# Performance work log

Hardware: AMD Instinct MI355X
Metric: run time of the kernel (lower is better)

The kernel has to match this reference:

```python
import jax, jax.numpy as jnp
import numpy as np

L, B, D, H, P = 4096, 4, 1024, 16, 256
HD = D // H
EPS = 1e-5


def _layer_norm(x, g, b):
    m = jnp.mean(x, axis=-1, keepdims=True)
    v = jnp.mean(jnp.square(x - m), axis=-1, keepdims=True)
    return (x - m) / jnp.sqrt(v + EPS) * g + b


def setup_inputs() -> dict:
    key = jax.random.key(0)
    ks = jax.random.split(key, 8)
    w = lambda k, shape: jax.random.normal(k, shape, jnp.float32) * 0.02
    return {
        "query": jax.random.normal(ks[0], (L, B, D), jnp.float32),
        "q_w": w(ks[1], (D, D)), "q_b": jnp.zeros((D,), jnp.float32),
        "k_w": w(ks[2], (D, D)), "k_b": jnp.zeros((D,), jnp.float32),
        "v_w": w(ks[3], (D, D)), "v_b": jnp.zeros((D,), jnp.float32),
        "e_weight": w(ks[4], (1, H, P, HD)),
        "e_out_w": w(ks[5], (D, D)), "e_out_b": jnp.zeros((D,), jnp.float32),
        "ln_g": jnp.ones((D,), jnp.float32), "ln_b": jnp.zeros((D,), jnp.float32),
        "out_w": w(ks[6], (D, D)), "out_b": jnp.zeros((D,), jnp.float32),
    }


def reference(query, q_w, q_b, k_w, k_b, v_w, v_b, e_weight,
              e_out_w, e_out_b, ln_g, ln_b, out_w, out_b):
    scaling = HD ** -0.5
    # ---- _compute_kv (kv_same=True, no padding mask) ----
    # kv: (L,B,D) -> (B,H,HD,L)
    kvh = query.reshape(L, B, H, HD).transpose(1, 2, 3, 0)
    # pkv = relu(E @ (kv * scaling)) : (B,H,P,L)
    pkv = jax.nn.relu(jnp.einsum('hpd,bhdl->bhpl', e_weight[0], kvh * scaling))
    # kv = pkv @ kv^T : (B,H,P,HD)
    kv = jnp.einsum('bhpl,bhdl->bhpd', pkv, kvh)
    # -> (P,B,D), e_out linear, residual add of e_weight, layer norm
    kv = kv.transpose(2, 0, 1, 3).reshape(P, B, D)
    kv = kv @ e_out_w.T + e_out_b
    kv = kv.reshape(P, B, H, HD) + e_weight.transpose(2, 0, 1, 3)  # broadcast (P,1,H,HD)
    kv = _layer_norm(kv.reshape(P, B, D), ln_g, ln_b)  # (P,B,D)

    # ---- standard MHA against the compressed kv ----
    q = (query @ q_w.T + q_b) * scaling            # (L,B,D)
    k = kv @ k_w.T + k_b                           # (P,B,D)
    v = kv @ v_w.T + v_b                           # (P,B,D)
    qh = q.reshape(L, B, H, HD)
    kh = k.reshape(P, B, H, HD)
    vh = v.reshape(P, B, H, HD)
    logits = jnp.einsum('lbhd,pbhd->bhlp', qh, kh)
    probs = jax.nn.softmax(logits, axis=-1)
    attn = jnp.einsum('bhlp,pbhd->lbhd', probs, vh).reshape(L, B, D)
    return attn @ out_w.T + out_b
```

## Files before the change

kernel.cpp:

```cpp
#include <hip/hip_runtime.h>
#include <hip/hip_bf16.h>
#include <cstdint>
#include <cstddef>

#define LL 4096
#define BB 4
#define DD 1024
#define HH 16
#define PP 256
#define HDD 64
#define LC 16
#define LCHUNK 256

constexpr float kScaling = 0.125f;
constexpr float kEps = 1e-5f;

typedef __attribute__((ext_vector_type(8))) short bf16x8;
typedef __attribute__((ext_vector_type(4))) short short4v;
typedef __attribute__((ext_vector_type(4))) float f32x4;

#define MFMA16(a, b, c) __builtin_amdgcn_mfma_f32_16x16x32_bf16((a), (b), (c), 0, 0, 0)

__device__ __forceinline__ unsigned short f2bf(float f) {
  unsigned int u = __builtin_bit_cast(unsigned int, f);
  u += 0x7FFFu + ((u >> 16) & 1u);
  return (unsigned short)(u >> 16);
}

__device__ __forceinline__ void gll16(const void* g, void* l) {
  __builtin_amdgcn_global_load_lds(
      (const __attribute__((address_space(1))) unsigned int*)g,
      (__attribute__((address_space(3))) unsigned int*)l, 16, 0, 0);
}

__global__ __launch_bounds__(256) void k_cvt(const float* __restrict__ src,
                                             unsigned short* __restrict__ dst,
                                             int n8) {
  int i = blockIdx.x * 256 + threadIdx.x;
  if (i >= n8) return;
  const float4* s = (const float4*)(src + (size_t)i * 8);
  float4 a = s[0], b = s[1];
  bf16x8 o;
  o[0] = f2bf(a.x); o[1] = f2bf(a.y); o[2] = f2bf(a.z); o[3] = f2bf(a.w);
  o[4] = f2bf(b.x); o[5] = f2bf(b.y); o[6] = f2bf(b.z); o[7] = f2bf(b.w);
  *(bf16x8*)(dst + (size_t)i * 8) = o;
}

__global__ __launch_bounds__(256) void k_compress_mfma(
    const unsigned short* __restrict__ qbf, const unsigned short* __restrict__ ewbf,
    float* __restrict__ parts) {
  const int bh = blockIdx.x, lc = blockIdx.y;
  const int b = bh >> 4, h = bh & 15;
  const int tid = threadIdx.x, wv = tid >> 6, lane = tid & 63;
  const int fr = lane & 15, fg = lane >> 4;

  __shared__ __align__(16) char Xl[8192];
  __shared__ __align__(16) char Xtl[8192];
  __shared__ __align__(16) char Pl[32768];

  bf16x8 ef[4][2];
#pragma unroll
  for (int pt = 0; pt < 4; ++pt)
#pragma unroll
    for (int kc = 0; kc < 2; ++kc)
      ef[pt][kc] = *(const bf16x8*)(ewbf +
          (size_t)((h * PP + wv * 64 + pt * 16 + fr) * HDD) + kc * 32 + fg * 8);

  f32x4 acc[4][4];
#pragma unroll
  for (int i = 0; i < 4; ++i)
#pragma unroll
    for (int j = 0; j < 4; ++j) acc[i][j] = (f32x4){0.f, 0.f, 0.f, 0.f};

  const int l0 = lc * LCHUNK;
  for (int t = 0; t < 4; ++t) {
    __syncthreads();
#pragma unroll
    for (int j = 0; j < 2; ++j) {
      int u = tid + j * 256;
      int l = u >> 3, c8 = u & 7;
      bf16x8 val = *(const bf16x8*)(qbf +
          ((size_t)(l0 + t * 64 + l) * BB + b) * DD + h * HDD + c8 * 8);
      *(bf16x8*)(Xl + l * 128 + ((c8 ^ (l & 7)) << 4)) = val;
#pragma unroll
      for (int i = 0; i < 8; ++i) {
        int dd = c8 * 8 + i;
        *(short*)(Xtl + dd * 128 + ((((l >> 3) ^ (dd & 7) ^ (dd >> 3)) & 7) << 4) +
                  ((l & 7) << 1)) = val[i];
      }
    }
    __syncthreads();
#pragma unroll
    for (int lt = 0; lt < 4; ++lt) {
      int rl = lt * 16 + fr;
      bf16x8 xa0 = *(const bf16x8*)(Xl + rl * 128 + (((0 + fg) ^ (rl & 7)) << 4));
      bf16x8 xa1 = *(const bf16x8*)(Xl + rl * 128 + (((4 + fg) ^ (rl & 7)) << 4));
#pragma unroll
      for (int pt = 0; pt < 4; ++pt) {
        f32x4 s = (f32x4){0.f, 0.f, 0.f, 0.f};
        s = MFMA16(xa0, ef[pt][0], s);
        s = MFMA16(xa1, ef[pt][1], s);
        short4v pk;
#pragma unroll
        for (int r = 0; r < 4; ++r)
          pk[r] = (short)f2bf(fmaxf(s[r] * kScaling, 0.f));
        int p = wv * 64 + pt * 16 + fr;
        int lbase = lt * 16 + fg * 4;
        int slot = lbase >> 3;
        *(short4v*)(Pl + p * 128 + ((slot ^ (p & 7)) << 4) + ((lbase & 7) << 1)) = pk;
      }
    }
    asm volatile("s_waitcnt lgkmcnt(0)" ::: "memory");
    __builtin_amdgcn_sched_barrier(0);
#pragma unroll
    for (int kc = 0; kc < 2; ++kc) {
      bf16x8 pa[4], xb[4];
#pragma unroll
      for (int pt = 0; pt < 4; ++pt) {
        int p = wv * 64 + pt * 16 + fr;
        pa[pt] = *(const bf16x8*)(Pl + p * 128 + (((kc * 4 + fg) ^ (p & 7)) << 4));
      }
#pragma unroll
      for (int dt = 0; dt < 4; ++dt) {
        int dd = dt * 16 + fr;
        xb[dt] = *(const bf16x8*)(Xtl + dd * 128 +
                  ((((kc * 4 + fg) ^ (dd & 7) ^ (dd >> 3)) & 7) << 4));
      }
#pragma unroll
      for (int pt = 0; pt < 4; ++pt)
#pragma unroll
        for (int dt = 0; dt < 4; ++dt)
          acc[pt][dt] = MFMA16(pa[pt], xb[dt], acc[pt][dt]);
    }
  }
  float* op = parts + (size_t)(lc * 64 + bh) * PP * HDD;
#pragma unroll
  for (int pt = 0; pt < 4; ++pt)
#pragma unroll
    for (int dt = 0; dt < 4; ++dt)
#pragma unroll
      for (int r = 0; r < 4; ++r) {
        int p = wv * 64 + pt * 16 + fg * 4 + r;
        int dd = dt * 16 + fr;
        op[(size_t)p * HDD + dd] = acc[pt][dt][r];
      }
}

__global__ __launch_bounds__(256) void k_reduce(const float* __restrict__ parts,
                                                unsigned short* __restrict__ kv_raw_bf) {
  int i = blockIdx.x * 256 + threadIdx.x;
  float s = 0.f;
#pragma unroll
  for (int lcc = 0; lcc < LC; ++lcc) s += parts[(size_t)lcc * (64 * PP * HDD) + i];
  int d = i & 63, p = (i >> 6) & 255, bh = i >> 14;
  int b = bh >> 4, h = bh & 15;
  kv_raw_bf[(size_t)(p * BB + b) * DD + h * HDD + d] = f2bf(s);
}

template <int MODE, typename OUTT>
__device__ __forceinline__ void gemm_body(
    const unsigned short* __restrict__ A, const unsigned short* __restrict__ W,
    const float* __restrict__ bias, const float* __restrict__ ew,
    OUTT* __restrict__ C, int m0, int n0, char* Al, char* Bl) {
  const int tid = threadIdx.x;
  const int wv = tid >> 6, lane = tid & 63;
  const int fr = lane & 15, fg = lane >> 4;
  const int wr = wv >> 1, wc = wv & 1;

  f32x4 acc[4][4];
#pragma unroll
  for (int i = 0; i < 4; ++i)
#pragma unroll
    for (int j = 0; j < 4; ++j) acc[i][j] = (f32x4){0.f, 0.f, 0.f, 0.f};

  for (int k0 = 0; k0 < DD; k0 += 64) {
    __syncthreads();
#pragma unroll
    for (int j = 0; j < 4; ++j) {
      int u = tid + j * 256;
      int row = u >> 3, slot = u & 7;
      size_t gcol = (size_t)(k0 + 8 * (slot ^ (row & 7)));
      gll16(A + (size_t)(m0 + row) * DD + gcol, Al + u * 16);
      gll16(W + (size_t)(n0 + row) * DD + gcol, Bl + u * 16);
    }
    __syncthreads();
#pragma unroll
    for (int kc = 0; kc < 2; ++kc) {
      bf16x8 af[4], bfr[4];
#pragma unroll
      for (int mt = 0; mt < 4; ++mt) {
        int r = wr * 64 + mt * 16 + fr;
        af[mt] = *(const bf16x8*)(Al + r * 128 + (((kc * 4 + fg) ^ (r & 7)) << 4));
      }
#pragma unroll
      for (int nt = 0; nt < 4; ++nt) {
        int r = wc * 64 + nt * 16 + fr;
        bfr[nt] = *(const bf16x8*)(Bl + r * 128 + (((kc * 4 + fg) ^ (r & 7)) << 4));
      }
#pragma unroll
      for (int mt = 0; mt < 4; ++mt)
#pragma unroll
        for (int nt = 0; nt < 4; ++nt)
          acc[mt][nt] = MFMA16(af[mt], bfr[nt], acc[mt][nt]);
    }
  }

  float bs[4];
#pragma unroll
  for (int nt = 0; nt < 4; ++nt) bs[nt] = bias[n0 + wc * 64 + nt * 16 + fr];
#pragma unroll
  for (int mt = 0; mt < 4; ++mt)
#pragma unroll
    for (int nt = 0; nt < 4; ++nt) {
      int n = n0 + wc * 64 + nt * 16 + fr;
#pragma unroll
      for (int r = 0; r < 4; ++r) {
        int m = m0 + wr * 64 + mt * 16 + fg * 4 + r;
        float v = acc[mt][nt][r] + bs[nt];
        if (MODE == 1) v *= kScaling;
        if (MODE == 2) {
          int p = m >> 2, hh = n >> 6, d2 = n & 63;
          v += ew[(size_t)((hh << 8) + p) * HDD + d2];
        }
        if constexpr (sizeof(OUTT) == 2)
          C[(size_t)m * DD + n] = (OUTT)f2bf(v);
        else
          C[(size_t)m * DD + n] = v;
      }
    }
}

template <int MODE, typename OUTT>
__global__ __launch_bounds__(256) void k_gemm_mfma(
    const unsigned short* __restrict__ A, const unsigned short* __restrict__ W,
    const float* __restrict__ bias, const float* __restrict__ ew,
    OUTT* __restrict__ C) {
  __shared__ __align__(16) char Al[16384];
  __shared__ __align__(16) char Bl[16384];
  gemm_body<MODE, OUTT>(A, W, bias, ew, C, blockIdx.x * 128, blockIdx.y * 128, Al, Bl);
}

__global__ __launch_bounds__(256) void k_gemm_kv(
    const unsigned short* __restrict__ A,
    const unsigned short* __restrict__ Wk, const unsigned short* __restrict__ Wv,
    const float* __restrict__ kb, const float* __restrict__ vb,
    unsigned short* __restrict__ Ck, unsigned short* __restrict__ Cv) {
  __shared__ __align__(16) char Al[16384];
  __shared__ __align__(16) char Bl[16384];
  if (blockIdx.z == 0)
    gemm_body<0, unsigned short>(A, Wk, kb, nullptr, Ck,
                                 blockIdx.x * 128, blockIdx.y * 128, Al, Bl);
  else
    gemm_body<0, unsigned short>(A, Wv, vb, nullptr, Cv,
                                 blockIdx.x * 128, blockIdx.y * 128, Al, Bl);
}

template <int MODE, typename OUTT>
__global__ __launch_bounds__(512, 2) void k_gemm256(
    const unsigned short* __restrict__ A, const unsigned short* __restrict__ W,
    const float* __restrict__ bias, OUTT* __restrict__ C) {
  __shared__ __align__(16) char lds[131072];
  const int tid = threadIdx.x;
  const int wv = tid >> 6, lane = tid & 63;
  const int fr = lane & 15, fg = lane >> 4;
  const int wm = wv >> 2, wn = wv & 3;
  const int m0 = blockIdx.x * 256, n0 = blockIdx.y * 256;
  const int srow = tid >> 2, sslot = tid & 3;

  auto stageHalf = [&](const unsigned short* __restrict__ G, int g0, int colbase,
                       int dstBase) {
#pragma unroll
    for (int j = 0; j < 2; ++j) {
      int row = srow + j * 128;
      int gs = sslot ^ ((row >> 1) & 3);
      gll16(G + (size_t)(g0 + row) * DD + colbase + gs * 8,
            lds + dstBase + (tid + j * 512) * 16);
    }
  };
  auto rdA = [&](int mf, int kc, int cb) -> bf16x8 {
    int r = wm * 128 + mf * 16 + fr;
    return *(const bf16x8*)(lds + cb + kc * 16384 + r * 64 +
                            ((fg ^ ((r >> 1) & 3)) << 4));
  };
  auto rdB = [&](int nf, int kc, int cb) -> bf16x8 {
    int r = wn * 64 + nf * 16 + fr;
    return *(const bf16x8*)(lds + cb + 32768 + kc * 16384 + r * 64 +
                            ((fg ^ ((r >> 1) & 3)) << 4));
  };

  f32x4 acc[8][4];
#pragma unroll
  for (int i = 0; i < 8; ++i)
#pragma unroll
    for (int j = 0; j < 4; ++j) acc[i][j] = (f32x4){0.f, 0.f, 0.f, 0.f};
  bf16x8 a[4], b[4];

  stageHalf(A, m0, 0, 0);
  stageHalf(W, n0, 0, 32768);
  stageHalf(A, m0, 32, 16384);
  stageHalf(W, n0, 32, 32768 + 16384);
  stageHalf(A, m0, 64, 65536);
  stageHalf(W, n0, 64, 65536 + 32768);
  asm volatile("s_waitcnt vmcnt(4)" ::: "memory");
  __builtin_amdgcn_s_barrier();

  const int NT = DD / 64;
  for (int t = 0; t < NT; ++t) {
    const int cb = (t & 1) << 16;
    const int nb = cb ^ 65536;
    const int k1 = (t + 1) * 64, k2 = (t + 2) * 64;

#pragma unroll
    for (int i = 0; i < 4; ++i) a[i] = rdA(i, 0, cb);
#pragma unroll
    for (int i = 0; i < 4; ++i) b[i] = rdB(i, 0, cb);
    if (t + 1 < NT) stageHalf(A, m0, k1 + 32, nb + 16384);
    __builtin_amdgcn_s_barrier();
    asm volatile("s_waitcnt lgkmcnt(0)" ::: "memory");
    __builtin_amdgcn_sched_barrier(0);
    __builtin_amdgcn_s_setprio(1);
#pragma unroll
    for (int mf = 0; mf < 4; ++mf)
#pragma unroll
      for (int nf = 0; nf < 4; ++nf)
        acc[mf][nf] = MFMA16(a[mf], b[nf], acc[mf][nf]);
    __builtin_amdgcn_s_setprio(0);
    __builtin_amdgcn_s_barrier();

#pragma unroll
    for (int i = 0; i < 4; ++i) a[i] = rdA(4 + i, 0, cb);
    if (t + 1 < NT) stageHalf(W, n0, k1 + 32, nb + 32768 + 16384);
    __builtin_amdgcn_s_barrier();
    asm volatile("s_waitcnt lgkmcnt(0)" ::: "memory");
    __builtin_amdgcn_sched_barrier(0);
    __builtin_amdgcn_s_setprio(1);
#pragma unroll
    for (int mf = 0; mf < 4; ++mf)
#pragma unroll
      for (int nf = 0; nf < 4; ++nf)
        acc[4 + mf][nf] = MFMA16(a[mf], b[nf], acc[4 + mf][nf]);
    __builtin_amdgcn_s_setprio(0);
    __builtin_amdgcn_s_barrier();

#pragma unroll
    for (int i = 0; i < 4; ++i) a[i] = rdA(i, 1, cb);
#pragma unroll
    for (int i = 0; i < 4; ++i) b[i] = rdB(i, 1, cb);
    if (t + 2 < NT) stageHalf(A, m0, k2, cb);
    __builtin_amdgcn_s_barrier();
    asm volatile("s_waitcnt lgkmcnt(0)" ::: "memory");
    __builtin_amdgcn_sched_barrier(0);
    __builtin_amdgcn_s_setprio(1);
#pragma unroll
    for (int mf = 0; mf < 4; ++mf)
#pragma unroll
      for (int nf = 0; nf < 4; ++nf)
        acc[mf][nf] = MFMA16(a[mf], b[nf], acc[mf][nf]);
    __builtin_amdgcn_s_setprio(0);
    __builtin_amdgcn_s_barrier();

#pragma unroll
    for (int i = 0; i < 4; ++i) a[i] = rdA(4 + i, 1, cb);
    if (t + 2 < NT) stageHalf(W, n0, k2, cb + 32768);
    __builtin_amdgcn_s_barrier();
    asm volatile("s_waitcnt lgkmcnt(0)" ::: "memory");
    __builtin_amdgcn_sched_barrier(0);
    __builtin_amdgcn_s_setprio(1);
#pragma unroll
    for (int mf = 0; mf < 4; ++mf)
#pragma unroll
      for (int nf = 0; nf < 4; ++nf)
        acc[4 + mf][nf] = MFMA16(a[mf], b[nf], acc[4 + mf][nf]);
    __builtin_amdgcn_s_setprio(0);
    if (t + 2 < NT) {
      asm volatile("s_waitcnt vmcnt(4)" ::: "memory");
    } else if (t + 1 < NT) {
      asm volatile("s_waitcnt vmcnt(0)" ::: "memory");
    }
    __builtin_amdgcn_s_barrier();
  }

  float bs[4];
#pragma unroll
  for (int nf = 0; nf < 4; ++nf) bs[nf] = bias[n0 + wn * 64 + nf * 16 + fr];
#pragma unroll
  for (int mf = 0; mf < 8; ++mf)
#pragma unroll
    for (int nf = 0; nf < 4; ++nf) {
      int n = n0 + wn * 64 + nf * 16 + fr;
#pragma unroll
      for (int r = 0; r < 4; ++r) {
        int m = m0 + wm * 128 + mf * 16 + fg * 4 + r;
        float v = acc[mf][nf][r] + bs[nf];
        if (MODE == 1) v *= kScaling;
        if constexpr (sizeof(OUTT) == 2)
          C[(size_t)m * DD + n] = (OUTT)f2bf(v);
        else
          C[(size_t)m * DD + n] = v;
      }
    }
}

__global__ __launch_bounds__(256) void k_ln(const float* __restrict__ x,
                                            const float* __restrict__ g,
                                            const float* __restrict__ bb,
                                            unsigned short* __restrict__ y) {
  const int r = blockIdx.x;
  const int tid = threadIdx.x;
  const float* xr = x + (size_t)r * DD;
  float4 v = *(const float4*)(xr + tid * 4);
  float s1 = v.x + v.y + v.z + v.w;
  float s2 = v.x * v.x + v.y * v.y + v.z * v.z + v.w * v.w;
#pragma unroll
  for (int off = 32; off > 0; off >>= 1) {
    s1 += __shfl_down(s1, off);
    s2 += __shfl_down(s2, off);
  }
  __shared__ float w1[4], w2[4];
  if ((tid & 63) == 0) { w1[tid >> 6] = s1; w2[tid >> 6] = s2; }
  __syncthreads();
  float S1 = w1[0] + w1[1] + w1[2] + w1[3];
  float S2 = w2[0] + w2[1] + w2[2] + w2[3];
  float mean = S1 * (1.f / DD);
  float var = S2 * (1.f / DD) - mean * mean;
  float rstd = rsqrtf(var + kEps);
  float4 gv = *(const float4*)(g + tid * 4);
  float4 bv = *(const float4*)(bb + tid * 4);
  short4v o;
  o[0] = (short)f2bf((v.x - mean) * rstd * gv.x + bv.x);
  o[1] = (short)f2bf((v.y - mean) * rstd * gv.y + bv.y);
  o[2] = (short)f2bf((v.z - mean) * rstd * gv.z + bv.z);
  o[3] = (short)f2bf((v.w - mean) * rstd * gv.w + bv.w);
  *(short4v*)(y + (size_t)r * DD + tid * 4) = o;
}

__global__ __launch_bounds__(512, 2) void k_attn_mfma(
    const unsigned short* __restrict__ qbf, const unsigned short* __restrict__ kbf,
    const unsigned short* __restrict__ vbf, unsigned short* __restrict__ attn) {
  const int bh = blockIdx.y;
  const int b = bh >> 4, h = bh & 15;
  const int tid = threadIdx.x, wv = tid >> 6, lane = tid & 63;
  const int fr = lane & 15, fg = lane >> 4;
  const int bl0 = blockIdx.x * 128;

  __shared__ __align__(16) char Kl[16384];
  __shared__ __align__(16) char Vt[16384];
  __shared__ __align__(16) char Pl[32768];

  const size_t qrow = ((size_t)(bl0 + wv * 16 + fr) * BB + b) * DD + h * HDD;
  bf16x8 qf0 = *(const bf16x8*)(qbf + qrow + fg * 8);
  bf16x8 qf1 = *(const bf16x8*)(qbf + qrow + 32 + fg * 8);

  f32x4 o[4];
#pragma unroll
  for (int dt = 0; dt < 4; ++dt) o[dt] = (f32x4){0.f, 0.f, 0.f, 0.f};
  float psum = 0.f;
  char* Pw = Pl + wv * 4096;

  for (int ph = 0; ph < 2; ++ph) {
    __syncthreads();
#pragma unroll
    for (int j = 0; j < 2; ++j) {
      int u = tid + j * 512;
      int p = u >> 3, slot = u & 7;
      gll16(kbf + ((size_t)((ph * 128 + p) * BB + b)) * DD + h * HDD +
                8 * (slot ^ (p & 7)),
            Kl + u * 16);
    }
#pragma unroll
    for (int j = 0; j < 2; ++j) {
      int u = tid + j * 512;
      int p = u >> 3, c8 = u & 7;
      bf16x8 val = *(const bf16x8*)(vbf +
          ((size_t)((ph * 128 + p) * BB + b)) * DD + h * HDD + c8 * 8);
      int pc = p >> 6, pl = p & 63;
#pragma unroll
      for (int i = 0; i < 8; ++i) {
        int dd = c8 * 8 + i;
        *(short*)(Vt + pc * 8192 + dd * 128 +
                  ((((pl >> 3) ^ (dd & 7) ^ (dd >> 3)) & 7) << 4) +
                  ((pl & 7) << 1)) = val[i];
      }
    }
    __syncthreads();

    f32x4 s[8];
    __builtin_amdgcn_s_setprio(1);
#pragma unroll
    for (int pt = 0; pt < 8; ++pt) {
      int pr = pt * 16 + fr;
      bf16x8 a0 = *(const bf16x8*)(Kl + pr * 128 + ((fg ^ (pr & 7)) << 4));
      bf16x8 a1 = *(const bf16x8*)(Kl + pr * 128 + (((4 + fg) ^ (pr & 7)) << 4));
      f32x4 acc = (f32x4){0.f, 0.f, 0.f, 0.f};
      acc = MFMA16(a0, qf0, acc);
      acc = MFMA16(a1, qf1, acc);
      s[pt] = acc;
    }
    __builtin_amdgcn_s_setprio(0);

#pragma unroll
    for (int pt = 0; pt < 8; ++pt) {
      float e0 = __expf(s[pt][0]), e1 = __expf(s[pt][1]);
      float e2 = __expf(s[pt][2]), e3 = __expf(s[pt][3]);
      psum += (e0 + e1) + (e2 + e3);
      short4v pk;
      pk[0] = (short)f2bf(e0); pk[1] = (short)f2bf(e1);
      pk[2] = (short)f2bf(e2); pk[3] = (short)f2bf(e3);
      int pbyte = (pt * 16 + fg * 4) * 2;
      int slot = pbyte >> 4, rem = pbyte & 15;
      *(short4v*)(Pw + fr * 256 + ((slot ^ (fr & 7)) << 4) + rem) = pk;
    }
    asm volatile("s_waitcnt lgkmcnt(0)" ::: "memory");
    __builtin_amdgcn_sched_barrier(0);

    __builtin_amdgcn_s_setprio(1);
#pragma unroll
    for (int kc = 0; kc < 4; ++kc) {
      int slot = kc * 4 + fg;
      bf16x8 pa = *(const bf16x8*)(Pw + fr * 256 + ((slot ^ (fr & 7)) << 4));
      int sl2 = (kc & 1) * 4 + fg;
#pragma unroll
      for (int dt = 0; dt < 4; ++dt) {
        int dd = dt * 16 + fr;
        bf16x8 vb = *(const bf16x8*)(Vt + (kc >> 1) * 8192 + dd * 128 +
                     (((sl2 ^ (dd & 7) ^ (dd >> 3)) & 7) << 4));
        o[dt] = MFMA16(pa, vb, o[dt]);
      }
    }
    __builtin_amdgcn_s_setprio(0);
  }

  psum += __shfl_xor(psum, 16);
  psum += __shfl_xor(psum, 32);

#pragma unroll
  for (int r = 0; r < 4; ++r) {
    int lloc = fg * 4 + r;
    float inv = 1.f / __shfl(psum, lloc);
    unsigned short* op = attn +
        ((size_t)(bl0 + wv * 16 + lloc) * BB + b) * DD + h * HDD;
#pragma unroll
    for (int dt = 0; dt < 4; ++dt)
      op[dt * 16 + fr] = f2bf(o[dt][r] * inv);
  }
}

extern "C" void kernel_launch(void* const* d_in, const int* in_sizes, int n_in,
                              void* d_out, int out_size, void* d_ws, size_t ws_size,
                              hipStream_t stream) {
  const float* query   = (const float*)d_in[0];
  const float* q_w     = (const float*)d_in[1];
  const float* q_b     = (const float*)d_in[2];
  const float* k_w     = (const float*)d_in[3];
  const float* k_b     = (const float*)d_in[4];
  const float* v_w     = (const float*)d_in[5];
  const float* v_b     = (const float*)d_in[6];
  const float* e_weight= (const float*)d_in[7];
  const float* e_out_w = (const float*)d_in[8];
  const float* e_out_b = (const float*)d_in[9];
  const float* ln_g    = (const float*)d_in[10];
  const float* ln_b    = (const float*)d_in[11];
  const float* out_w   = (const float*)d_in[12];
  const float* out_b   = (const float*)d_in[13];
  float* out = (float*)d_out;

  char* w = (char*)d_ws;
  float* parts            = (float*)w;
  unsigned short* q_bf    = (unsigned short*)w;
  unsigned short* attn_bf = (unsigned short*)(w + (32u << 20));
  unsigned short* query_bf= (unsigned short*)(w + (64u << 20));
  unsigned short* kv_raw  = (unsigned short*)(w + (96u << 20));
  float* kv_eo            = (float*)(w + (98u << 20));
  unsigned short* kv_ln   = (unsigned short*)(w + (102u << 20));
  unsigned short* k_buf   = (unsigned short*)(w + (104u << 20));
  unsigned short* v_buf   = (unsigned short*)(w + (106u << 20));
  unsigned short* wq  = (unsigned short*)(w + (108u << 20));
  unsigned short* wk  = (unsigned short*)(w + (110u << 20));
  unsigned short* wv_ = (unsigned short*)(w + (112u << 20));
  unsigned short* weo = (unsigned short*)(w + (114u << 20));
  unsigned short* wo  = (unsigned short*)(w + (116u << 20));
  unsigned short* ewb = (unsigned short*)(w + (118u << 20));

  k_cvt<<<8192, 256, 0, stream>>>(query, query_bf, 2097152);
  k_cvt<<<512, 256, 0, stream>>>(q_w, wq, 131072);
  k_cvt<<<512, 256, 0, stream>>>(k_w, wk, 131072);
  k_cvt<<<512, 256, 0, stream>>>(v_w, wv_, 131072);
  k_cvt<<<512, 256, 0, stream>>>(e_out_w, weo, 131072);
  k_cvt<<<512, 256, 0, stream>>>(out_w, wo, 131072);
  k_cvt<<<128, 256, 0, stream>>>(e_weight, ewb, 32768);

  k_compress_mfma<<<dim3(64, LC), 256, 0, stream>>>(query_bf, ewb, parts);
  k_reduce<<<4096, 256, 0, stream>>>(parts, kv_raw);
  k_gemm_mfma<2, float><<<dim3(8, 8), 256, 0, stream>>>(kv_raw, weo, e_out_b, e_weight, kv_eo);
  k_ln<<<PP * BB, 256, 0, stream>>>(kv_eo, ln_g, ln_b, kv_ln);
  k_gemm256<1, unsigned short><<<dim3(64, 4), 512, 0, stream>>>(query_bf, wq, q_b, q_bf);
  k_gemm_kv<<<dim3(8, 8, 2), 256, 0, stream>>>(kv_ln, wk, wv_, k_b, v_b, k_buf, v_buf);
  k_attn_mfma<<<dim3(32, 64), 512, 0, stream>>>(q_bf, k_buf, v_buf, attn_bf);
  k_gemm256<0, float><<<dim3(64, 4), 512, 0, stream>>>(attn_bf, wo, out_b, out);
}
```

Measured before the change: 238.1 us.

## Merge conversion kernels, store compress partials in bf16, double attention rows per block

All six fp32-to-bf16 conversion launches are merged into one kernel that dispatches on thread index, which removes launch overhead. The compress kernel's per-chunk partial sums are now written in bf16 instead of fp32, halving write and reduce traffic at the cost of extra rounding in a 16-way sum. The attention kernel now processes 256 query rows per block, so each staged K/V tile is reused for two sets of 128 rows. The grid is halved to match, which leaves fewer blocks to spread across the GPU.

```diff
diff --git a/kernel.cpp b/kernel.cpp
--- a/kernel.cpp
+++ b/kernel.cpp
@@ -26,6 +26,9 @@
   u += 0x7FFFu + ((u >> 16) & 1u);
   return (unsigned short)(u >> 16);
 }
+__device__ __forceinline__ float bf2f(unsigned short u) {
+  return __builtin_bit_cast(float, ((unsigned int)u) << 16);
+}
 
 __device__ __forceinline__ void gll16(const void* g, void* l) {
   __builtin_amdgcn_global_load_lds(
@@ -33,22 +36,38 @@
       (__attribute__((address_space(3))) unsigned int*)l, 16, 0, 0);
 }
 
-__global__ __launch_bounds__(256) void k_cvt(const float* __restrict__ src,
-                                             unsigned short* __restrict__ dst,
-                                             int n8) {
+__global__ __launch_bounds__(256) void k_cvt_all(
+    const float* __restrict__ q,
+    const float* __restrict__ w0, const float* __restrict__ w1,
+    const float* __restrict__ w2, const float* __restrict__ w3,
+    const float* __restrict__ w4, const float* __restrict__ w5,
+    unsigned short* __restrict__ dq,
+    unsigned short* __restrict__ d0, unsigned short* __restrict__ d1,
+    unsigned short* __restrict__ d2, unsigned short* __restrict__ d3,
+    unsigned short* __restrict__ d4, unsigned short* __restrict__ d5) {
   int i = blockIdx.x * 256 + threadIdx.x;
-  if (i >= n8) return;
-  const float4* s = (const float4*)(src + (size_t)i * 8);
+  const float* src; unsigned short* dst; int off;
+  if (i < 2097152) { src = q; dst = dq; off = i; }
+  else {
+    int j = i - 2097152; int w = j >> 17; off = j & 131071;
+    if (w == 0) { src = w0; dst = d0; }
+    else if (w == 1) { src = w1; dst = d1; }
+    else if (w == 2) { src = w2; dst = d2; }
+    else if (w == 3) { src = w3; dst = d3; }
+    else if (w == 4) { src = w4; dst = d4; }
+    else { if (off >= 32768) return; src = w5; dst = d5; }
+  }
+  const float4* s = (const float4*)(src + (size_t)off * 8);
   float4 a = s[0], b = s[1];
   bf16x8 o;
   o[0] = f2bf(a.x); o[1] = f2bf(a.y); o[2] = f2bf(a.z); o[3] = f2bf(a.w);
   o[4] = f2bf(b.x); o[5] = f2bf(b.y); o[6] = f2bf(b.z); o[7] = f2bf(b.w);
-  *(bf16x8*)(dst + (size_t)i * 8) = o;
+  *(bf16x8*)(dst + (size_t)off * 8) = o;
 }
 
 __global__ __launch_bounds__(256) void k_compress_mfma(
     const unsigned short* __restrict__ qbf, const unsigned short* __restrict__ ewbf,
-    float* __restrict__ parts) {
+    unsigned short* __restrict__ parts) {
   const int bh = blockIdx.x, lc = blockIdx.y;
   const int b = bh >> 4, h = bh & 15;
   const int tid = threadIdx.x, wv = tid >> 6, lane = tid & 63;
@@ -133,7 +152,7 @@
           acc[pt][dt] = MFMA16(pa[pt], xb[dt], acc[pt][dt]);
     }
   }
-  float* op = parts + (size_t)(lc * 64 + bh) * PP * HDD;
+  unsigned short* op = parts + (size_t)(lc * 64 + bh) * PP * HDD;
 #pragma unroll
   for (int pt = 0; pt < 4; ++pt)
 #pragma unroll
@@ -142,16 +161,16 @@
       for (int r = 0; r < 4; ++r) {
         int p = wv * 64 + pt * 16 + fg * 4 + r;
         int dd = dt * 16 + fr;
-        op[(size_t)p * HDD + dd] = acc[pt][dt][r];
-      }
-}
-
-__global__ __launch_bounds__(256) void k_reduce(const float* __restrict__ parts,
+        op[(size_t)p * HDD + dd] = f2bf(acc[pt][dt][r]);
+      }
+}
+
+__global__ __launch_bounds__(256) void k_reduce(const unsigned short* __restrict__ parts,
                                                 unsigned short* __restrict__ kv_raw_bf) {
   int i = blockIdx.x * 256 + threadIdx.x;
   float s = 0.f;
 #pragma unroll
-  for (int lcc = 0; lcc < LC; ++lcc) s += parts[(size_t)lcc * (64 * PP * HDD) + i];
+  for (int lcc = 0; lcc < LC; ++lcc) s += bf2f(parts[(size_t)lcc * (64 * PP * HDD) + i]);
   int d = i & 63, p = (i >> 6) & 255, bh = i >> 14;
   int b = bh >> 4, h = bh & 15;
   kv_raw_bf[(size_t)(p * BB + b) * DD + h * HDD + d] = f2bf(s);
@@ -441,20 +460,26 @@
   const int b = bh >> 4, h = bh & 15;
   const int tid = threadIdx.x, wv = tid >> 6, lane = tid & 63;
   const int fr = lane & 15, fg = lane >> 4;
-  const int bl0 = blockIdx.x * 128;
+  const int bl0 = blockIdx.x * 256;
 
   __shared__ __align__(16) char Kl[16384];
   __shared__ __align__(16) char Vt[16384];
   __shared__ __align__(16) char Pl[32768];
 
-  const size_t qrow = ((size_t)(bl0 + wv * 16 + fr) * BB + b) * DD + h * HDD;
-  bf16x8 qf0 = *(const bf16x8*)(qbf + qrow + fg * 8);
-  bf16x8 qf1 = *(const bf16x8*)(qbf + qrow + 32 + fg * 8);
-
-  f32x4 o[4];
-#pragma unroll
-  for (int dt = 0; dt < 4; ++dt) o[dt] = (f32x4){0.f, 0.f, 0.f, 0.f};
-  float psum = 0.f;
+  bf16x8 qf[2][2];
+#pragma unroll
+  for (int ql = 0; ql < 2; ++ql) {
+    const size_t qrow = ((size_t)(bl0 + ql * 128 + wv * 16 + fr) * BB + b) * DD + h * HDD;
+    qf[ql][0] = *(const bf16x8*)(qbf + qrow + fg * 8);
+    qf[ql][1] = *(const bf16x8*)(qbf + qrow + 32 + fg * 8);
+  }
+
+  f32x4 o[2][4];
+#pragma unroll
+  for (int ql = 0; ql < 2; ++ql)
+#pragma unroll
+    for (int dt = 0; dt < 4; ++dt) o[ql][dt] = (f32x4){0.f, 0.f, 0.f, 0.f};
+  float psum[2] = {0.f, 0.f};
   char* Pw = Pl + wv * 4096;
 
   for (int ph = 0; ph < 2; ++ph) {
@@ -484,64 +509,72 @@
     }
     __syncthreads();
 
-    f32x4 s[8];
-    __builtin_amdgcn_s_setprio(1);
-#pragma unroll
-    for (int pt = 0; pt < 8; ++pt) {
-      int pr = pt * 16 + fr;
-      bf16x8 a0 = *(const bf16x8*)(Kl + pr * 128 + ((fg ^ (pr & 7)) << 4));
-      bf16x8 a1 = *(const bf16x8*)(Kl + pr * 128 + (((4 + fg) ^ (pr & 7)) << 4));
-      f32x4 acc = (f32x4){0.f, 0.f, 0.f, 0.f};
-      acc = MFMA16(a0, qf0, acc);
-      acc = MFMA16(a1, qf1, acc);
-      s[pt] = acc;
-    }
-    __builtin_amdgcn_s_setprio(0);
-
-#pragma unroll
-    for (int pt = 0; pt < 8; ++pt) {
-      float e0 = __expf(s[pt][0]), e1 = __expf(s[pt][1]);
-      float e2 = __expf(s[pt][2]), e3 = __expf(s[pt][3]);
-      psum += (e0 + e1) + (e2 + e3);
-      short4v pk;
-      pk[0] = (short)f2bf(e0); pk[1] = (short)f2bf(e1);
-      pk[2] = (short)f2bf(e2); pk[3] = (short)f2bf(e3);
-      int pbyte = (pt * 16 + fg * 4) * 2;
-      int slot = pbyte >> 4, rem = pbyte & 15;
-      *(short4v*)(Pw + fr * 256 + ((slot ^ (fr & 7)) << 4) + rem) = pk;
-    }
-    asm volatile("s_waitcnt lgkmcnt(0)" ::: "memory");
-    __builtin_amdgcn_sched_barrier(0);
-
-    __builtin_amdgcn_s_setprio(1);
-#pragma unroll
-    for (int kc = 0; kc < 4; ++kc) {
-      int slot = kc * 4 + fg;
-      bf16x8 pa = *(const bf16x8*)(Pw + fr * 256 + ((slot ^ (fr & 7)) << 4));
-      int sl2 = (kc & 1) * 4 + fg;
-#pragma unroll
-      for (int dt = 0; dt < 4; ++dt) {
-        int dd = dt * 16 + fr;
-        bf16x8 vb = *(const bf16x8*)(Vt + (kc >> 1) * 8192 + dd * 128 +
-                     (((sl2 ^ (dd & 7) ^ (dd >> 3)) & 7) << 4));
-        o[dt] = MFMA16(pa, vb, o[dt]);
-      }
-    }
-    __builtin_amdgcn_s_setprio(0);
-  }
-
-  psum += __shfl_xor(psum, 16);
-  psum += __shfl_xor(psum, 32);
-
-#pragma unroll
-  for (int r = 0; r < 4; ++r) {
-    int lloc = fg * 4 + r;
-    float inv = 1.f / __shfl(psum, lloc);
-    unsigned short* op = attn +
-        ((size_t)(bl0 + wv * 16 + lloc) * BB + b) * DD + h * HDD;
-#pragma unroll
-    for (int dt = 0; dt < 4; ++dt)
-      op[dt * 16 + fr] = f2bf(o[dt][r] * inv);
+#pragma unroll
+    for (int ql = 0; ql < 2; ++ql) {
+      f32x4 s[8];
+      __builtin_amdgcn_s_setprio(1);
+#pragma unroll
+      for (int pt = 0; pt < 8; ++pt) {
+        int pr = pt * 16 + fr;
+        bf16x8 a0 = *(const bf16x8*)(Kl + pr * 128 + ((fg ^ (pr & 7)) << 4));
+        bf16x8 a1 = *(const bf16x8*)(Kl + pr * 128 + (((4 + fg) ^ (pr & 7)) << 4));
+        f32x4 acc = (f32x4){0.f, 0.f, 0.f, 0.f};
+        acc = MFMA16(a0, qf[ql][0], acc);
+        acc = MFMA16(a1, qf[ql][1], acc);
+        s[pt] = acc;
+      }
+      __builtin_amdgcn_s_setprio(0);
+
+      asm volatile("s_waitcnt lgkmcnt(0)" ::: "memory");
+      __builtin_amdgcn_sched_barrier(0);
+#pragma unroll
+      for (int pt = 0; pt < 8; ++pt) {
+        float e0 = __expf(s[pt][0]), e1 = __expf(s[pt][1]);
+        float e2 = __expf(s[pt][2]), e3 = __expf(s[pt][3]);
+        psum[ql] += (e0 + e1) + (e2 + e3);
+        short4v pk;
+        pk[0] = (short)f2bf(e0); pk[1] = (short)f2bf(e1);
+        pk[2] = (short)f2bf(e2); pk[3] = (short)f2bf(e3);
+        int pbyte = (pt * 16 + fg * 4) * 2;
+        int slot = pbyte >> 4, rem = pbyte & 15;
+        *(short4v*)(Pw + fr * 256 + ((slot ^ (fr & 7)) << 4) + rem) = pk;
+      }
+      asm volatile("s_waitcnt lgkmcnt(0)" ::: "memory");
+      __builtin_amdgcn_sched_barrier(0);
+
+      __builtin_amdgcn_s_setprio(1);
+#pragma unroll
+      for (int kc = 0; kc < 4; ++kc) {
+        int slot = kc * 4 + fg;
+        bf16x8 pa = *(const bf16x8*)(Pw + fr * 256 + ((slot ^ (fr & 7)) << 4));
+        int sl2 = (kc & 1) * 4 + fg;
+#pragma unroll
+        for (int dt = 0; dt < 4; ++dt) {
+          int dd = dt * 16 + fr;
+          bf16x8 vb = *(const bf16x8*)(Vt + (kc >> 1) * 8192 + dd * 128 +
+                       (((sl2 ^ (dd & 7) ^ (dd >> 3)) & 7) << 4));
+          o[ql][dt] = MFMA16(pa, vb, o[ql][dt]);
+        }
+      }
+      __builtin_amdgcn_s_setprio(0);
+    }
+  }
+
+#pragma unroll
+  for (int ql = 0; ql < 2; ++ql) {
+    float ps = psum[ql];
+    ps += __shfl_xor(ps, 16);
+    ps += __shfl_xor(ps, 32);
+#pragma unroll
+    for (int r = 0; r < 4; ++r) {
+      int lloc = fg * 4 + r;
+      float inv = 1.f / __shfl(ps, lloc);
+      unsigned short* op = attn +
+          ((size_t)(bl0 + ql * 128 + wv * 16 + lloc) * BB + b) * DD + h * HDD;
+#pragma unroll
+      for (int dt = 0; dt < 4; ++dt)
+        op[dt * 16 + fr] = f2bf(o[ql][dt][r] * inv);
+    }
   }
 }
 
@@ -565,7 +598,7 @@
   float* out = (float*)d_out;
 
   char* w = (char*)d_ws;
-  float* parts            = (float*)w;
+  unsigned short* parts   = (unsigned short*)w;
   unsigned short* q_bf    = (unsigned short*)w;
   unsigned short* attn_bf = (unsigned short*)(w + (32u << 20));
   unsigned short* query_bf= (unsigned short*)(w + (64u << 20));
@@ -581,13 +614,8 @@
   unsigned short* wo  = (unsigned short*)(w + (116u << 20));
   unsigned short* ewb = (unsigned short*)(w + (118u << 20));
 
-  k_cvt<<<8192, 256, 0, stream>>>(query, query_bf, 2097152);
-  k_cvt<<<512, 256, 0, stream>>>(q_w, wq, 131072);
-  k_cvt<<<512, 256, 0, stream>>>(k_w, wk, 131072);
-  k_cvt<<<512, 256, 0, stream>>>(v_w, wv_, 131072);
-  k_cvt<<<512, 256, 0, stream>>>(e_out_w, weo, 131072);
-  k_cvt<<<512, 256, 0, stream>>>(out_w, wo, 131072);
-  k_cvt<<<128, 256, 0, stream>>>(e_weight, ewb, 32768);
+  k_cvt_all<<<10880, 256, 0, stream>>>(query, q_w, k_w, v_w, e_out_w, out_w, e_weight,
+                                       query_bf, wq, wk, wv_, weo, wo, ewb);
 
   k_compress_mfma<<<dim3(64, LC), 256, 0, stream>>>(query_bf, ewb, parts);
   k_reduce<<<4096, 256, 0, stream>>>(parts, kv_raw);
@@ -595,6 +623,6 @@
   k_ln<<<PP * BB, 256, 0, stream>>>(kv_eo, ln_g, ln_b, kv_ln);
   k_gemm256<1, unsigned short><<<dim3(64, 4), 512, 0, stream>>>(query_bf, wq, q_b, q_bf);
   k_gemm_kv<<<dim3(8, 8, 2), 256, 0, stream>>>(kv_ln, wk, wv_, k_b, v_b, k_buf, v_buf);
-  k_attn_mfma<<<dim3(32, 64), 512, 0, stream>>>(q_bf, k_buf, v_buf, attn_bf);
+  k_attn_mfma<<<dim3(16, 64), 512, 0, stream>>>(q_bf, k_buf, v_buf, attn_bf);
   k_gemm256<0, float><<<dim3(64, 4), 512, 0, stream>>>(attn_bf, wo, out_b, out);
 }
```

New measurement: 222.3 us. 6.6% less time.
